# Optimization experiments

Hardware: AMD Instinct MI355X
Metric: run time of the kernel (lower is better)

Reference implementation:

```python
import jax, jax.numpy as jnp
import numpy as np

N, E, D, C = 100000, 640000, 128, 4


def setup_inputs() -> dict:
    key = jax.random.key(0)
    ks = jax.random.split(key, 8)
    s = 1.0 / np.sqrt(D)
    return {
        "x": jax.random.normal(ks[0], (N, D), jnp.float32),
        "edge_index": jax.random.randint(ks[1], (2, E), 0, N),
        "edge_attr": jax.random.normal(ks[2], (E, D), jnp.float32),
        "masks": jax.random.uniform(ks[3], (C, N), jnp.float32),
        "W1": jax.random.normal(ks[4], (C, D, D), jnp.float32) * s,
        "b1": jnp.zeros((C, D), jnp.float32),
        "W2": jax.random.normal(ks[5], (C, D, D), jnp.float32) * s,
        "b2": jnp.zeros((C, D), jnp.float32),
        "eps": jnp.zeros((C,), jnp.float32),
        "gamma": jnp.ones((C, D), jnp.float32),
        "beta": jnp.zeros((C, D), jnp.float32),
        "run_mean": jnp.zeros((C, D), jnp.float32),
        "run_var": jnp.ones((C, D), jnp.float32),
    }


def reference(x, edge_index, edge_attr, masks, W1, b1, W2, b2, eps, gamma, beta, run_mean, run_var):
    BN_EPS = 1e-5
    src, dst = edge_index[0], edge_index[1]
    x_in = x
    for c in range(C):
        # GINEConv: sum_{j->i} relu(x_j + e_ij), then (1+eps)*x_i + agg -> MLP
        msg = jax.nn.relu(x[src] + edge_attr)                      # [E, D]
        agg = jax.ops.segment_sum(msg, dst, num_segments=x.shape[0])
        h = (1.0 + eps[c]) * x + agg
        h = jax.nn.relu(h @ W1[c] + b1[c]) @ W2[c] + b2[c]
        # masked sublayer residual
        x = masks[c][:, None] * h + x
        # BatchNorm1d (eval mode, running stats)
        x = (x - run_mean[c]) * jax.lax.rsqrt(run_var[c] + BN_EPS) * gamma[c] + beta[c]
    # final relu (dropout is identity in eval) + outer residual
    return x_in + jax.nn.relu(x)
```

## Files before the change

kernel.cpp:

```cpp
#include <hip/hip_runtime.h>
#include <cstddef>

#define D 128
#define CHUNK 1024
#define BM 64
#define LDSH 136

typedef __attribute__((ext_vector_type(8))) short s16x8;
typedef __attribute__((ext_vector_type(8))) unsigned short u16x8;
typedef __attribute__((ext_vector_type(4))) float f32x4;
typedef __attribute__((ext_vector_type(2))) float f32x2;

__device__ __forceinline__ unsigned short f2bf(float f) {
  unsigned u = __builtin_bit_cast(unsigned, f);
  u += 0x7FFFu + ((u >> 16) & 1u);
  return (unsigned short)(u >> 16);
}
__device__ __forceinline__ float bf2f(unsigned short h) {
  unsigned u = ((unsigned)h) << 16;
  return __builtin_bit_cast(float, u);
}
__device__ __forceinline__ unsigned f32x4_to_fp8(float4 v) {
  int r = __builtin_amdgcn_cvt_pk_fp8_f32(v.x, v.y, 0, false);
  r = __builtin_amdgcn_cvt_pk_fp8_f32(v.z, v.w, r, true);
  return (unsigned)r;
}
__device__ __forceinline__ void fp8x4_to_f32(unsigned u, float* o) {
  f32x2 lo = __builtin_amdgcn_cvt_pk_f32_fp8((int)u, false);
  f32x2 hi = __builtin_amdgcn_cvt_pk_f32_fp8((int)u, true);
  o[0] = lo[0]; o[1] = lo[1]; o[2] = hi[0]; o[3] = hi[1];
}

__global__ __launch_bounds__(256) void hist_kernel(const int* __restrict__ ei,
                                                   int* __restrict__ deg, int E) {
  int e = blockIdx.x * 256 + threadIdx.x;
  if (e < E) atomicAdd(&deg[ei[E + e]], 1);
}

__global__ __launch_bounds__(256) void partial_kernel(const int* __restrict__ deg,
                                                      int* __restrict__ partial, int N) {
  __shared__ int s[256];
  int base = blockIdx.x * CHUNK;
  int sum = 0;
  for (int j = threadIdx.x; j < CHUNK; j += 256) {
    int idx = base + j;
    sum += (idx < N) ? deg[idx] : 0;
  }
  s[threadIdx.x] = sum;
  __syncthreads();
  for (int ofs = 128; ofs > 0; ofs >>= 1) {
    if (threadIdx.x < ofs) s[threadIdx.x] += s[threadIdx.x + ofs];
    __syncthreads();
  }
  if (threadIdx.x == 0) partial[blockIdx.x] = s[0];
}

__global__ __launch_bounds__(1024) void scanpart_kernel(int* partial, int nb) {
  __shared__ int s[1024];
  int tid = threadIdx.x;
  int v = (tid < nb) ? partial[tid] : 0;
  s[tid] = v;
  __syncthreads();
  for (int o = 1; o < 1024; o <<= 1) {
    int t = (tid >= o) ? s[tid - o] : 0;
    __syncthreads();
    s[tid] += t;
    __syncthreads();
  }
  if (tid < nb) partial[tid] = s[tid] - v;
}

__global__ __launch_bounds__(256) void chunkscan_kernel(const int* __restrict__ deg,
                                                        const int* __restrict__ partial,
                                                        int* __restrict__ off, int N) {
  __shared__ int ws[4];
  int base = blockIdx.x * CHUNK;
  int i0 = base + threadIdx.x * 4;
  int d[4];
  int s = 0;
#pragma unroll
  for (int k = 0; k < 4; ++k) {
    d[k] = (i0 + k < N) ? deg[i0 + k] : 0;
    s += d[k];
  }
  int lane = threadIdx.x & 63;
  int incl = s;
  for (int o = 1; o < 64; o <<= 1) {
    int v = __shfl_up(incl, o, 64);
    if (lane >= o) incl += v;
  }
  int wave = threadIdx.x >> 6;
  if (lane == 63) ws[wave] = incl;
  __syncthreads();
  int wofs = 0;
  for (int w = 0; w < wave; ++w) wofs += ws[w];
  int run = partial[blockIdx.x] + wofs + (incl - s);
#pragma unroll
  for (int k = 0; k < 4; ++k) {
    int idx = i0 + k;
    if (idx < N) {
      off[idx] = run;
      run += d[k];
      if (idx == N - 1) off[N] = run;
    }
  }
}

__global__ __launch_bounds__(256) void scatter_conv_kernel(
    const int* __restrict__ ei, const float* __restrict__ ea,
    const int* __restrict__ off, int* __restrict__ cursor,
    int* __restrict__ sperm, unsigned char* __restrict__ eap, int E) {
  int t = blockIdx.x * 256 + threadIdx.x;
  int lane = t & 31;
  int e = t >> 5;
  if (e >= E) return;
  int p = 0;
  if (lane == 0) {
    int dnode = ei[E + e];
    p = off[dnode] + atomicAdd(&cursor[dnode], 1);
    sperm[p] = ei[e];
  }
  p = __shfl(p, 0, 32);
  float4 v = *reinterpret_cast<const float4*>(ea + (size_t)e * D + lane * 4);
  reinterpret_cast<unsigned*>(eap)[(size_t)p * 32 + lane] = f32x4_to_fp8(v);
}

__global__ __launch_bounds__(256) void conv_x_kernel(const float* __restrict__ x,
                                                     unsigned short* __restrict__ xbf,
                                                     long long n8) {
  long long t = (long long)blockIdx.x * 256 + threadIdx.x;
  if (t >= n8) return;
  float4 v0 = reinterpret_cast<const float4*>(x)[t * 2];
  float4 v1 = reinterpret_cast<const float4*>(x)[t * 2 + 1];
  ushort4 o0, o1;
  o0.x = f2bf(v0.x); o0.y = f2bf(v0.y); o0.z = f2bf(v0.z); o0.w = f2bf(v0.w);
  o1.x = f2bf(v1.x); o1.y = f2bf(v1.y); o1.z = f2bf(v1.z); o1.w = f2bf(v1.w);
  reinterpret_cast<ushort4*>(xbf)[t * 2] = o0;
  reinterpret_cast<ushort4*>(xbf)[t * 2 + 1] = o1;
}

__global__ void pack_w_kernel(const float* __restrict__ W1, const float* __restrict__ W2,
                              unsigned short* __restrict__ pk) {
  int c = blockIdx.x;
  const float* Ws[2] = {W1 + (size_t)c * D * D, W2 + (size_t)c * D * D};
  unsigned short* base = pk + (size_t)c * 2 * D * D;
  for (int t = threadIdx.x; t < 2048; t += blockDim.x) {
    int ct = t >> 8, ks = (t >> 6) & 3, l = t & 63;
    int col = ct * 16 + (l & 15);
    int krow = ks * 32 + ((l >> 4) & 3) * 8;
    for (int w = 0; w < 2; ++w) {
      unsigned short* dst = base + (size_t)w * D * D;
      const float* W = Ws[w];
      for (int i = 0; i < 8; ++i)
        dst[(size_t)t * 8 + i] = f2bf(W[(size_t)(krow + i) * D + col]);
    }
  }
}

__global__ __launch_bounds__(256, 5) void layer_kernel(
    const float* __restrict__ x, const unsigned short* __restrict__ xbf,
    const unsigned char* __restrict__ eap,
    const int* __restrict__ off, const int* __restrict__ sperm,
    const float* __restrict__ epsp,
    const unsigned short* __restrict__ wpk,
    const float* __restrict__ b1, const float* __restrict__ b2,
    const float* __restrict__ mask,
    const float* __restrict__ gamma, const float* __restrict__ beta,
    const float* __restrict__ rmean, const float* __restrict__ rvar,
    const float* __restrict__ x_in, float* __restrict__ out,
    unsigned short* __restrict__ xbf_out,
    int N, int is_last) {
  __shared__ __align__(16) unsigned short smem[BM * LDSH];
  unsigned short* h_s = smem;
  unsigned short* t_s = smem;
  unsigned short* y_s = smem;

  const int tid = threadIdx.x;
  const int r0 = blockIdx.x * BM;
  const float one_eps = 1.0f + epsp[0];

  {
    const int qw = tid >> 4;
    const int l16 = tid & 15;
#pragma unroll
    for (int it = 0; it < 4; ++it) {
      int row = it * 16 + qw;
      int gr = r0 + row;
      unsigned short* ph = h_s + row * LDSH + l16 * 8;
      if (gr >= N) {
        u16x8 z = {0, 0, 0, 0, 0, 0, 0, 0};
        *reinterpret_cast<u16x8*>(ph) = z;
        continue;
      }
      int beg = off[gr], end = off[gr + 1];
      float acc[8] = {0.f, 0.f, 0.f, 0.f, 0.f, 0.f, 0.f, 0.f};
      for (int i = beg; i < end; i += 8) {
        int n = end - i;
        int idx[8], sidx[8];
#pragma unroll
        for (int k = 0; k < 8; ++k) idx[k] = (k < n) ? i + k : i;
#pragma unroll
        for (int k = 0; k < 8; ++k) sidx[k] = sperm[idx[k]];
        u16x8 xv[8];
        uint2 eu[8];
#pragma unroll
        for (int k = 0; k < 8; ++k) {
          xv[k] = *reinterpret_cast<const u16x8*>(xbf + (size_t)sidx[k] * D + l16 * 8);
          eu[k] = *reinterpret_cast<const uint2*>(eap + (size_t)idx[k] * D + l16 * 8);
        }
#pragma unroll
        for (int k = 0; k < 8; ++k) {
          if (k == 0 || k < n) {
            float ev[8];
            fp8x4_to_f32(eu[k].x, ev);
            fp8x4_to_f32(eu[k].y, ev + 4);
#pragma unroll
            for (int q = 0; q < 8; ++q)
              acc[q] += fmaxf(bf2f((unsigned short)xv[k][q]) + ev[q], 0.f);
          }
        }
      }
      const float* xd = x + (size_t)gr * D + l16 * 8;
      float4 x0 = *reinterpret_cast<const float4*>(xd);
      float4 x1 = *reinterpret_cast<const float4*>(xd + 4);
      float hv[8];
      hv[0] = fmaf(one_eps, x0.x, acc[0]); hv[1] = fmaf(one_eps, x0.y, acc[1]);
      hv[2] = fmaf(one_eps, x0.z, acc[2]); hv[3] = fmaf(one_eps, x0.w, acc[3]);
      hv[4] = fmaf(one_eps, x1.x, acc[4]); hv[5] = fmaf(one_eps, x1.y, acc[5]);
      hv[6] = fmaf(one_eps, x1.z, acc[6]); hv[7] = fmaf(one_eps, x1.w, acc[7]);
      u16x8 hi8;
#pragma unroll
      for (int q = 0; q < 8; ++q) hi8[q] = f2bf(hv[q]);
      *reinterpret_cast<u16x8*>(ph) = hi8;
    }
  }
  __syncthreads();

  const int l = tid & 63;
  const int wave = tid >> 6;
  const int wm = wave >> 1;
  const int wn = wave & 1;
  const int cl = l & 15;
  const int kq = l >> 4;

  f32x4 acc1[2][4];
  {
    s16x8 a[2][4];
#pragma unroll
    for (int rt = 0; rt < 2; ++rt) {
      int row = wm * 32 + rt * 16 + cl;
#pragma unroll
      for (int ks = 0; ks < 4; ++ks)
        a[rt][ks] = *reinterpret_cast<const s16x8*>(h_s + row * LDSH + ks * 32 + kq * 8);
    }
    const s16x8* w1 = reinterpret_cast<const s16x8*>(wpk);
#pragma unroll
    for (int ct = 0; ct < 4; ++ct) {
      int gct = wn * 4 + ct;
      f32x4 a0 = {0.f, 0.f, 0.f, 0.f};
      f32x4 a1 = {0.f, 0.f, 0.f, 0.f};
#pragma unroll
      for (int ks = 0; ks < 4; ++ks) {
        s16x8 bh = w1[(gct * 4 + ks) * 64 + l];
        a0 = __builtin_amdgcn_mfma_f32_16x16x32_bf16(a[0][ks], bh, a0, 0, 0, 0);
        a1 = __builtin_amdgcn_mfma_f32_16x16x32_bf16(a[1][ks], bh, a1, 0, 0, 0);
      }
      acc1[0][ct] = a0;
      acc1[1][ct] = a1;
    }
  }
  __syncthreads();

#pragma unroll
  for (int ct = 0; ct < 4; ++ct) {
    int gct = wn * 4 + ct;
    float bv = b1[gct * 16 + cl];
#pragma unroll
    for (int i = 0; i < 4; ++i) {
      t_s[(wm * 32 + kq * 4 + i) * LDSH + gct * 16 + cl] = f2bf(fmaxf(acc1[0][ct][i] + bv, 0.f));
      t_s[(wm * 32 + 16 + kq * 4 + i) * LDSH + gct * 16 + cl] = f2bf(fmaxf(acc1[1][ct][i] + bv, 0.f));
    }
  }
  __syncthreads();

  f32x4 acc2[2][4];
  {
    s16x8 a[2][4];
#pragma unroll
    for (int rt = 0; rt < 2; ++rt) {
      int row = wm * 32 + rt * 16 + cl;
#pragma unroll
      for (int ks = 0; ks < 4; ++ks)
        a[rt][ks] = *reinterpret_cast<const s16x8*>(t_s + row * LDSH + ks * 32 + kq * 8);
    }
    const s16x8* w2 = reinterpret_cast<const s16x8*>(wpk + D * D);
#pragma unroll
    for (int ct = 0; ct < 4; ++ct) {
      int gct = wn * 4 + ct;
      f32x4 a0 = {0.f, 0.f, 0.f, 0.f};
      f32x4 a1 = {0.f, 0.f, 0.f, 0.f};
#pragma unroll
      for (int ks = 0; ks < 4; ++ks) {
        s16x8 bh = w2[(gct * 4 + ks) * 64 + l];
        a0 = __builtin_amdgcn_mfma_f32_16x16x32_bf16(a[0][ks], bh, a0, 0, 0, 0);
        a1 = __builtin_amdgcn_mfma_f32_16x16x32_bf16(a[1][ks], bh, a1, 0, 0, 0);
      }
      acc2[0][ct] = a0;
      acc2[1][ct] = a1;
    }
  }
  __syncthreads();

#pragma unroll
  for (int ct = 0; ct < 4; ++ct) {
    int gct = wn * 4 + ct;
#pragma unroll
    for (int i = 0; i < 4; ++i) {
      y_s[(wm * 32 + kq * 4 + i) * LDSH + gct * 16 + cl] = f2bf(acc2[0][ct][i]);
      y_s[(wm * 32 + 16 + kq * 4 + i) * LDSH + gct * 16 + cl] = f2bf(acc2[1][ct][i]);
    }
  }
  __syncthreads();

  for (int j = tid; j < BM * 16; j += 256) {
    int row = j >> 4, c8 = j & 15;
    int gr = r0 + row;
    if (gr >= N) continue;
    u16x8 yb = *reinterpret_cast<const u16x8*>(y_s + row * LDSH + c8 * 8);
    float mk = mask[gr];
    const float* xp = x + (size_t)gr * D + c8 * 8;
    float4 xv0 = *reinterpret_cast<const float4*>(xp);
    float4 xv1 = *reinterpret_cast<const float4*>(xp + 4);
    float xs[8] = {xv0.x, xv0.y, xv0.z, xv0.w, xv1.x, xv1.y, xv1.z, xv1.w};
    float vo[8];
#pragma unroll
    for (int q = 0; q < 8; ++q) {
      int col = c8 * 8 + q;
      float yv = bf2f((unsigned short)yb[q]);
      float v = fmaf(mk, yv + b2[col], xs[q]);
      v = fmaf(v - rmean[col], gamma[col] * rsqrtf(rvar[col] + 1e-5f), beta[col]);
      vo[q] = v;
    }
    if (is_last) {
      const float* xip = x_in + (size_t)gr * D + c8 * 8;
      float4 xi0 = *reinterpret_cast<const float4*>(xip);
      float4 xi1 = *reinterpret_cast<const float4*>(xip + 4);
      float xi[8] = {xi0.x, xi0.y, xi0.z, xi0.w, xi1.x, xi1.y, xi1.z, xi1.w};
#pragma unroll
      for (int q = 0; q < 8; ++q) vo[q] = xi[q] + fmaxf(vo[q], 0.f);
    } else {
      u16x8 o;
#pragma unroll
      for (int q = 0; q < 8; ++q) o[q] = f2bf(vo[q]);
      *reinterpret_cast<u16x8*>(xbf_out + (size_t)gr * D + c8 * 8) = o;
    }
    float4 w0 = make_float4(vo[0], vo[1], vo[2], vo[3]);
    float4 w1 = make_float4(vo[4], vo[5], vo[6], vo[7]);
    float* op = out + (size_t)gr * D + c8 * 8;
    *reinterpret_cast<float4*>(op) = w0;
    *reinterpret_cast<float4*>(op + 4) = w1;
  }
}

static inline char* align_up(char* p, size_t a) {
  return (char*)(((size_t)p + a - 1) & ~(a - 1));
}

extern "C" void kernel_launch(void* const* d_in, const int* in_sizes, int n_in,
                              void* d_out, int out_size, void* d_ws, size_t ws_size,
                              hipStream_t stream) {
  const float* x_in  = (const float*)d_in[0];
  const int*   ei    = (const int*)d_in[1];
  const float* ea    = (const float*)d_in[2];
  const float* masks = (const float*)d_in[3];
  const float* W1    = (const float*)d_in[4];
  const float* b1    = (const float*)d_in[5];
  const float* W2    = (const float*)d_in[6];
  const float* b2    = (const float*)d_in[7];
  const float* eps   = (const float*)d_in[8];
  const float* gamma = (const float*)d_in[9];
  const float* beta  = (const float*)d_in[10];
  const float* rmean = (const float*)d_in[11];
  const float* rvar  = (const float*)d_in[12];
  const int N = in_sizes[0] / D;
  const int E = in_sizes[1] / 2;
  const int C = in_sizes[8];
  const int nb = (N + CHUNK - 1) / CHUNK;

  char* w = (char*)d_ws;
  float* xalt  = (float*)w;  w += (size_t)N * D * sizeof(float);
  int* deg     = (int*)w;    w += (size_t)N * sizeof(int);
  int* off     = (int*)w;    w += (size_t)(N + 1) * sizeof(int);
  int* cursor  = (int*)w;    w += (size_t)N * sizeof(int);
  int* partial = (int*)w;    w += (size_t)(nb + 1) * sizeof(int);
  int* sperm   = (int*)w;    w += (size_t)E * sizeof(int);
  w = align_up(w, 128);
  unsigned short* xbfA = (unsigned short*)w;  w += (size_t)N * D * sizeof(unsigned short);
  unsigned short* xbfB = (unsigned short*)w;  w += (size_t)N * D * sizeof(unsigned short);
  unsigned short* wpk  = (unsigned short*)w;  w += (size_t)C * 2 * D * D * sizeof(unsigned short);
  w = align_up(w, 128);
  unsigned char* eap = (unsigned char*)w;

  hipMemsetAsync(deg, 0, (size_t)N * sizeof(int), stream);
  hipMemsetAsync(cursor, 0, (size_t)N * sizeof(int), stream);
  hist_kernel<<<(E + 255) / 256, 256, 0, stream>>>(ei, deg, E);
  partial_kernel<<<nb, 256, 0, stream>>>(deg, partial, N);
  scanpart_kernel<<<1, 1024, 0, stream>>>(partial, nb);
  chunkscan_kernel<<<nb, 256, 0, stream>>>(deg, partial, off, N);
  scatter_conv_kernel<<<(E + 7) / 8, 256, 0, stream>>>(ei, ea, off, cursor, sperm, eap, E);
  pack_w_kernel<<<C, 256, 0, stream>>>(W1, W2, wpk);
  long long n8 = (long long)N * D / 8;
  conv_x_kernel<<<(int)((n8 + 255) / 256), 256, 0, stream>>>(x_in, xbfA, n8);

  const int blocks = (N + BM - 1) / BM;
  const float* xc = x_in;
  const unsigned short* xbf_cur = xbfA;
  for (int c = 0; c < C; ++c) {
    float* dst = (((C - 1 - c) & 1) == 0) ? (float*)d_out : xalt;
    unsigned short* xbf_next = (xbf_cur == xbfA) ? xbfB : xbfA;
    layer_kernel<<<blocks, 256, 0, stream>>>(
        xc, xbf_cur, eap, off, sperm, eps + c,
        wpk + (size_t)c * 2 * D * D,
        b1 + (size_t)c * D, b2 + (size_t)c * D,
        masks + (size_t)c * N,
        gamma + (size_t)c * D, beta + (size_t)c * D,
        rmean + (size_t)c * D, rvar + (size_t)c * D,
        x_in, dst, xbf_next, N, (c == C - 1) ? 1 : 0);
    xc = dst;
    xbf_cur = xbf_next;
  }
}
```

Before: 503.2 us.

## Keep layer state in bf16 only and precompute folded BatchNorm scale/shift

Result: faster. 439.4 us (-12.7%).

```diff
diff --git a/kernel.cpp b/kernel.cpp
--- a/kernel.cpp
+++ b/kernel.cpp
@@ -140,10 +140,19 @@
 }
 
 __global__ void pack_w_kernel(const float* __restrict__ W1, const float* __restrict__ W2,
-                              unsigned short* __restrict__ pk) {
+                              const float* __restrict__ gamma, const float* __restrict__ beta,
+                              const float* __restrict__ rmean, const float* __restrict__ rvar,
+                              unsigned short* __restrict__ pk,
+                              float* __restrict__ bnsc, float* __restrict__ bnbb) {
   int c = blockIdx.x;
   const float* Ws[2] = {W1 + (size_t)c * D * D, W2 + (size_t)c * D * D};
   unsigned short* base = pk + (size_t)c * 2 * D * D;
+  if (threadIdx.x < D) {
+    int col = threadIdx.x;
+    float sc = gamma[(size_t)c * D + col] * rsqrtf(rvar[(size_t)c * D + col] + 1e-5f);
+    bnsc[(size_t)c * D + col] = sc;
+    bnbb[(size_t)c * D + col] = beta[(size_t)c * D + col] - rmean[(size_t)c * D + col] * sc;
+  }
   for (int t = threadIdx.x; t < 2048; t += blockDim.x) {
     int ct = t >> 8, ks = (t >> 6) & 3, l = t & 63;
     int col = ct * 16 + (l & 15);
@@ -158,15 +167,14 @@
 }
 
 __global__ __launch_bounds__(256, 5) void layer_kernel(
-    const float* __restrict__ x, const unsigned short* __restrict__ xbf,
+    const unsigned short* __restrict__ xbf,
     const unsigned char* __restrict__ eap,
     const int* __restrict__ off, const int* __restrict__ sperm,
     const float* __restrict__ epsp,
     const unsigned short* __restrict__ wpk,
     const float* __restrict__ b1, const float* __restrict__ b2,
     const float* __restrict__ mask,
-    const float* __restrict__ gamma, const float* __restrict__ beta,
-    const float* __restrict__ rmean, const float* __restrict__ rvar,
+    const float* __restrict__ bnsc, const float* __restrict__ bnbb,
     const float* __restrict__ x_in, float* __restrict__ out,
     unsigned short* __restrict__ xbf_out,
     int N, int is_last) {
@@ -220,17 +228,11 @@
           }
         }
       }
-      const float* xd = x + (size_t)gr * D + l16 * 8;
-      float4 x0 = *reinterpret_cast<const float4*>(xd);
-      float4 x1 = *reinterpret_cast<const float4*>(xd + 4);
-      float hv[8];
-      hv[0] = fmaf(one_eps, x0.x, acc[0]); hv[1] = fmaf(one_eps, x0.y, acc[1]);
-      hv[2] = fmaf(one_eps, x0.z, acc[2]); hv[3] = fmaf(one_eps, x0.w, acc[3]);
-      hv[4] = fmaf(one_eps, x1.x, acc[4]); hv[5] = fmaf(one_eps, x1.y, acc[5]);
-      hv[6] = fmaf(one_eps, x1.z, acc[6]); hv[7] = fmaf(one_eps, x1.w, acc[7]);
+      u16x8 xo = *reinterpret_cast<const u16x8*>(xbf + (size_t)gr * D + l16 * 8);
       u16x8 hi8;
 #pragma unroll
-      for (int q = 0; q < 8; ++q) hi8[q] = f2bf(hv[q]);
+      for (int q = 0; q < 8; ++q)
+        hi8[q] = f2bf(fmaf(one_eps, bf2f((unsigned short)xo[q]), acc[q]));
       *reinterpret_cast<u16x8*>(ph) = hi8;
     }
   }
@@ -327,19 +329,25 @@
     int gr = r0 + row;
     if (gr >= N) continue;
     u16x8 yb = *reinterpret_cast<const u16x8*>(y_s + row * LDSH + c8 * 8);
+    u16x8 xr = *reinterpret_cast<const u16x8*>(xbf + (size_t)gr * D + c8 * 8);
     float mk = mask[gr];
-    const float* xp = x + (size_t)gr * D + c8 * 8;
-    float4 xv0 = *reinterpret_cast<const float4*>(xp);
-    float4 xv1 = *reinterpret_cast<const float4*>(xp + 4);
-    float xs[8] = {xv0.x, xv0.y, xv0.z, xv0.w, xv1.x, xv1.y, xv1.z, xv1.w};
+    const float* b2p = b2 + c8 * 8;
+    const float* scp = bnsc + c8 * 8;
+    const float* bbp = bnbb + c8 * 8;
+    float4 b20 = *reinterpret_cast<const float4*>(b2p);
+    float4 b21 = *reinterpret_cast<const float4*>(b2p + 4);
+    float4 sc0 = *reinterpret_cast<const float4*>(scp);
+    float4 sc1 = *reinterpret_cast<const float4*>(scp + 4);
+    float4 bb0 = *reinterpret_cast<const float4*>(bbp);
+    float4 bb1 = *reinterpret_cast<const float4*>(bbp + 4);
+    float b2a[8] = {b20.x, b20.y, b20.z, b20.w, b21.x, b21.y, b21.z, b21.w};
+    float sca[8] = {sc0.x, sc0.y, sc0.z, sc0.w, sc1.x, sc1.y, sc1.z, sc1.w};
+    float bba[8] = {bb0.x, bb0.y, bb0.z, bb0.w, bb1.x, bb1.y, bb1.z, bb1.w};
     float vo[8];
 #pragma unroll
     for (int q = 0; q < 8; ++q) {
-      int col = c8 * 8 + q;
-      float yv = bf2f((unsigned short)yb[q]);
-      float v = fmaf(mk, yv + b2[col], xs[q]);
-      v = fmaf(v - rmean[col], gamma[col] * rsqrtf(rvar[col] + 1e-5f), beta[col]);
-      vo[q] = v;
+      float v = fmaf(mk, bf2f((unsigned short)yb[q]) + b2a[q], bf2f((unsigned short)xr[q]));
+      vo[q] = fmaf(v, sca[q], bba[q]);
     }
     if (is_last) {
       const float* xip = x_in + (size_t)gr * D + c8 * 8;
@@ -348,17 +356,17 @@
       float xi[8] = {xi0.x, xi0.y, xi0.z, xi0.w, xi1.x, xi1.y, xi1.z, xi1.w};
 #pragma unroll
       for (int q = 0; q < 8; ++q) vo[q] = xi[q] + fmaxf(vo[q], 0.f);
+      float4 w0 = make_float4(vo[0], vo[1], vo[2], vo[3]);
+      float4 w1 = make_float4(vo[4], vo[5], vo[6], vo[7]);
+      float* op = out + (size_t)gr * D + c8 * 8;
+      *reinterpret_cast<float4*>(op) = w0;
+      *reinterpret_cast<float4*>(op + 4) = w1;
     } else {
       u16x8 o;
 #pragma unroll
       for (int q = 0; q < 8; ++q) o[q] = f2bf(vo[q]);
       *reinterpret_cast<u16x8*>(xbf_out + (size_t)gr * D + c8 * 8) = o;
     }
-    float4 w0 = make_float4(vo[0], vo[1], vo[2], vo[3]);
-    float4 w1 = make_float4(vo[4], vo[5], vo[6], vo[7]);
-    float* op = out + (size_t)gr * D + c8 * 8;
-    *reinterpret_cast<float4*>(op) = w0;
-    *reinterpret_cast<float4*>(op + 4) = w1;
   }
 }
 
@@ -388,7 +396,6 @@
   const int nb = (N + CHUNK - 1) / CHUNK;
 
   char* w = (char*)d_ws;
-  float* xalt  = (float*)w;  w += (size_t)N * D * sizeof(float);
   int* deg     = (int*)w;    w += (size_t)N * sizeof(int);
   int* off     = (int*)w;    w += (size_t)(N + 1) * sizeof(int);
   int* cursor  = (int*)w;    w += (size_t)N * sizeof(int);
@@ -398,6 +405,8 @@
   unsigned short* xbfA = (unsigned short*)w;  w += (size_t)N * D * sizeof(unsigned short);
   unsigned short* xbfB = (unsigned short*)w;  w += (size_t)N * D * sizeof(unsigned short);
   unsigned short* wpk  = (unsigned short*)w;  w += (size_t)C * 2 * D * D * sizeof(unsigned short);
+  float* bnsc = (float*)w;   w += (size_t)C * D * sizeof(float);
+  float* bnbb = (float*)w;   w += (size_t)C * D * sizeof(float);
   w = align_up(w, 128);
   unsigned char* eap = (unsigned char*)w;
 
@@ -408,25 +417,21 @@
   scanpart_kernel<<<1, 1024, 0, stream>>>(partial, nb);
   chunkscan_kernel<<<nb, 256, 0, stream>>>(deg, partial, off, N);
   scatter_conv_kernel<<<(E + 7) / 8, 256, 0, stream>>>(ei, ea, off, cursor, sperm, eap, E);
-  pack_w_kernel<<<C, 256, 0, stream>>>(W1, W2, wpk);
+  pack_w_kernel<<<C, 256, 0, stream>>>(W1, W2, gamma, beta, rmean, rvar, wpk, bnsc, bnbb);
   long long n8 = (long long)N * D / 8;
   conv_x_kernel<<<(int)((n8 + 255) / 256), 256, 0, stream>>>(x_in, xbfA, n8);
 
   const int blocks = (N + BM - 1) / BM;
-  const float* xc = x_in;
   const unsigned short* xbf_cur = xbfA;
   for (int c = 0; c < C; ++c) {
-    float* dst = (((C - 1 - c) & 1) == 0) ? (float*)d_out : xalt;
     unsigned short* xbf_next = (xbf_cur == xbfA) ? xbfB : xbfA;
     layer_kernel<<<blocks, 256, 0, stream>>>(
-        xc, xbf_cur, eap, off, sperm, eps + c,
+        xbf_cur, eap, off, sperm, eps + c,
         wpk + (size_t)c * 2 * D * D,
         b1 + (size_t)c * D, b2 + (size_t)c * D,
         masks + (size_t)c * N,
-        gamma + (size_t)c * D, beta + (size_t)c * D,
-        rmean + (size_t)c * D, rvar + (size_t)c * D,
-        x_in, dst, xbf_next, N, (c == C - 1) ? 1 : 0);
-    xc = dst;
+        bnsc + (size_t)c * D, bnbb + (size_t)c * D,
+        x_in, (float*)d_out, xbf_next, N, (c == C - 1) ? 1 : 0);
     xbf_cur = xbf_next;
   }
 }
```
